# Kernel optimization log

Measured on AMD Instinct MI355X. Metric: run time of the kernel, lower is better.

Reference implementation:

```python
import jax, jax.numpy as jnp
import numpy as np

# Dims: B=batch, H=query heads, HKV=kv heads, T=query len, S=cache/key len, Dh=head dim
B, H, HKV, T, S, Dh = 2, 32, 8, 1024, 2048, 128
THRESH = 0.000488  # keep keys whose mean attention (over heads and queries) exceeds this


def setup_inputs() -> dict:
    key = jax.random.key(0)
    k1, k2, k3 = jax.random.split(key, 3)
    # attn_w emulates post-softmax attention probabilities: rows sum to 1 over key axis
    attn_w = jax.random.uniform(k1, (B, H, T, S), dtype=jnp.float32)
    attn_w = attn_w / attn_w.sum(axis=-1, keepdims=True)
    v = jax.random.normal(k2, (B, HKV, S, Dh), dtype=jnp.float32)
    w_o = jax.random.normal(k3, (H * Dh, H * Dh), dtype=jnp.float32) * 0.02  # o_proj weight (no bias, Mistral)
    return {"attn_w": attn_w, "v": v, "w_o": w_o}


def reference(attn_w, v, w_o):
    # keep = attn_w.mean(dim=(1,2)) > thresh  -> [B, S]
    keep = attn_w.mean(axis=(1, 2)) > THRESH
    pruned_weights = attn_w * keep[:, None, None, :].astype(attn_w.dtype)  # [B,H,T,S]
    # repeat_kv: [B,HKV,S,Dh] -> [B,H,S,Dh] via repeat_interleave on head axis
    groups = attn_w.shape[1] // v.shape[1]
    v_full = jnp.repeat(v, groups, axis=1)
    new_ctx = jnp.einsum('bhts,bhsd->bhtd', pruned_weights, v_full)  # [B,H,T,Dh]
    Bn, Hn, Tn, Dn = new_ctx.shape
    new_ctx = new_ctx.transpose(0, 2, 1, 3).reshape(Bn, Tn, Hn * Dn)  # [B,T,H*Dh]
    out = new_ctx @ w_o.T  # o_proj
    return (out, pruned_weights)
```

## Files before the change

kernel.cpp:

```cpp
#include <hip/hip_runtime.h>
#include <hip/hip_bf16.h>

#define B_ 2
#define H_ 32
#define HKV_ 8
#define T_ 1024
#define S_ 2048
#define DH_ 128
#define HD_ 4096
#define NROW_ 32768
#define THRESH_D 0.000488

typedef __attribute__((ext_vector_type(4))) float f32x4;
typedef __attribute__((ext_vector_type(8))) short bf16x8;

#define SCHED0() __builtin_amdgcn_sched_barrier(0)

__device__ __forceinline__ void gload_lds16(const void* g, void* l) {
  __builtin_amdgcn_global_load_lds(
      (const __attribute__((address_space(1))) void*)g,
      (__attribute__((address_space(3))) void*)l, 16, 0, 0);
}


__global__ void reduce_wo_k(const double* __restrict__ partial,
                            float* __restrict__ keep,
                            const float* __restrict__ w,
                            __hip_bfloat16* __restrict__ wb) {
  __shared__ double sh[4][64];
  if (blockIdx.x < 64) {
    int b = blockIdx.x >> 5;
    int s0 = (blockIdx.x & 31) * 64;
    int wv = threadIdx.x >> 6, l = threadIdx.x & 63;
    const double* p = partial + (size_t)b * 256 * S_ + s0 + l;
    double sum = 0.0;
    #pragma unroll 8
    for (int y = 0; y < 64; ++y) sum += p[(size_t)(wv * 64 + y) * S_];
    sh[wv][l] = sum;
    __syncthreads();
    if (wv == 0) {
      double t = (sh[0][l] + sh[1][l]) + (sh[2][l] + sh[3][l]);
      keep[b * S_ + s0 + l] = (t * (1.0 / 32768.0) > THRESH_D) ? 1.0f : 0.0f;
    }
  } else {
    size_t idx = ((size_t)(blockIdx.x - 64) * 256 + threadIdx.x) * 8;
    int n = (int)(idx >> 12);
    int k0 = (int)(idx & (HD_ - 1));
    float4 x = *(const float4*)(w + idx);
    float4 y = *(const float4*)(w + idx + 4);
    union { bf16x8 v8; __hip_bfloat16 h[8]; } u;
    u.h[0] = __float2bfloat16(x.x); u.h[1] = __float2bfloat16(x.y);
    u.h[2] = __float2bfloat16(x.z); u.h[3] = __float2bfloat16(x.w);
    u.h[4] = __float2bfloat16(y.x); u.h[5] = __float2bfloat16(y.y);
    u.h[6] = __float2bfloat16(y.z); u.h[7] = __float2bfloat16(y.w);
    int ksw = (k0 & ~63) | ((k0 ^ ((n & 7) << 3)) & 63);
    *(bf16x8*)(wb + (size_t)n * HD_ + ksw) = u.v8;
  }
}


#define BK2 64
#define NS2 64

__global__ __launch_bounds__(512) void gemm2_k(
    const __hip_bfloat16* __restrict__ Actx,
    const __hip_bfloat16* __restrict__ Bw,
    float* __restrict__ out) {
  __shared__ __align__(16) __hip_bfloat16 As[2][128 * BK2];
  __shared__ __align__(16) __hip_bfloat16 Bs[2][128 * BK2];
  int tid = threadIdx.x;
  int lg = ((blockIdx.x & 7) << 6) | (blockIdx.x >> 3);
  int n0 = (lg >> 4) * 128;
  int m0 = (lg & 15) * 128;
  const __hip_bfloat16* Ap = Actx + (size_t)m0 * HD_;
  const __hip_bfloat16* Bp = Bw + (size_t)n0 * HD_;
  int wave = tid >> 6, lane = tid & 63;
  int l16 = lane & 15, lk = lane >> 4;

  f32x4 acc[8];
  f32x4 z = {0.f, 0.f, 0.f, 0.f};
  #pragma unroll
  for (int n = 0; n < 8; ++n) acc[n] = z;

  auto issue = [&](int ks, int buf) {
    const __hip_bfloat16* ga = Ap + (size_t)(tid >> 3) * HD_ + ks * BK2 + (tid & 7) * 8;
    const __hip_bfloat16* gb = Bp + (size_t)(tid >> 3) * HD_ + ks * BK2 + (tid & 7) * 8;
    char* la = (char*)&As[buf][0] + tid * 16;
    char* lb = (char*)&Bs[buf][0] + tid * 16;
    gload_lds16(ga, la);
    gload_lds16(ga + (size_t)64 * HD_, la + 8192);
    gload_lds16(gb, lb);
    gload_lds16(gb + (size_t)64 * HD_, lb + 8192);
  };

  auto mfmaStep = [&](int buf) {
    char* ab = (char*)&As[buf][0];
    char* bb = (char*)&Bs[buf][0];
    #pragma unroll
    for (int kk = 0; kk < 2; ++kk) {
      int kb = kk * 64 + lk * 16;
      int ar = wave * 16 + l16;
      bf16x8 af = *(const bf16x8*)(ab + (ar * 128 + (kb ^ ((ar & 7) << 4))));
      #pragma unroll
      for (int n = 0; n < 8; ++n) {
        int br = n * 16 + l16;
        bf16x8 bf = *(const bf16x8*)(bb + (br * 128 + (kb ^ ((br & 7) << 4))));
        acc[n] = __builtin_amdgcn_mfma_f32_16x16x32_bf16(af, bf, acc[n], 0, 0, 0);
      }
    }
  };

  issue(0, 0);
  for (int ks = 0; ks < NS2; ++ks) {
    int cur = ks & 1;
    if (ks + 1 < NS2) issue(ks + 1, cur ^ 1);
    SCHED0();
    if (ks + 1 < NS2) {
      asm volatile("s_waitcnt vmcnt(4) lgkmcnt(0)" ::: "memory");
    } else {
      asm volatile("s_waitcnt vmcnt(0) lgkmcnt(0)" ::: "memory");
    }
    SCHED0();
    __builtin_amdgcn_s_barrier();
    SCHED0();
    mfmaStep(cur);
    SCHED0();
    __builtin_amdgcn_s_barrier();
    SCHED0();
  }

  #pragma unroll
  for (int n = 0; n < 8; ++n)
    #pragma unroll
    for (int r = 0; r < 4; ++r) {
      int row = m0 + wave * 16 + lk * 4 + r;
      int col = n0 + n * 16 + l16;
      out[(size_t)row * HD_ + col] = acc[n][r];
    }
}


__global__ __launch_bounds__(256) void colsumA_k(
    const float* __restrict__ attn, double* __restrict__ partial,
    __hip_bfloat16* __restrict__ abf) {
  int tid = threadIdx.x;
  int chunk = blockIdx.x;
  size_t base = (size_t)chunk * 128 * S_;
  const float* ap = attn + base;
  __hip_bfloat16* ob = abf + base;
  double a0 = 0, a1 = 0, a2 = 0, a3 = 0;
  double b0 = 0, b1 = 0, b2 = 0, b3 = 0;
  #pragma unroll 4
  for (int i = 0; i < 256; ++i) {
    size_t off = (size_t)i * 1024 + tid * 4;
    f32x4 vv = *(const f32x4*)(ap + off);
    int row = i >> 1;
    int s = ((i & 1) << 10) + tid * 4;
    int ssw = (s & ~63) | ((s ^ ((row & 7) << 3)) & 63);
    union { ushort4 u4; __hip_bfloat16 h[4]; } u;
    u.h[0] = __float2bfloat16(vv.x); u.h[1] = __float2bfloat16(vv.y);
    u.h[2] = __float2bfloat16(vv.z); u.h[3] = __float2bfloat16(vv.w);
    *(ushort4*)(ob + (size_t)row * S_ + ssw) = u.u4;
    if (i & 1) { b0 += vv.x; b1 += vv.y; b2 += vv.z; b3 += vv.w; }
    else       { a0 += vv.x; a1 += vv.y; a2 += vv.z; a3 += vv.w; }
  }
  double* o = partial + (size_t)chunk * S_ + tid * 4;
  o[0] = a0; o[1] = a1; o[2] = a2; o[3] = a3;
  double* o2 = partial + (size_t)chunk * S_ + 1024 + tid * 4;
  o2[0] = b0; o2[1] = b1; o2[2] = b2; o2[3] = b3;
}

__global__ void convert_vA_k(const float* __restrict__ v,
                             const float* __restrict__ keep,
                             __hip_bfloat16* __restrict__ vt) {
  __shared__ float tile[32][33];
  int bh = blockIdx.z;
  int b = bh >> 3;
  int s0 = blockIdx.x * 32, d0 = blockIdx.y * 32;
  const float* vp = v + (size_t)bh * (S_ * DH_);
  __hip_bfloat16* vtp = vt + (size_t)bh * (S_ * DH_);
  int tx = threadIdx.x, ty = threadIdx.y;
  for (int i = 0; i < 32; i += 8)
    tile[ty + i][tx] = vp[(size_t)(s0 + ty + i) * DH_ + d0 + tx];
  __syncthreads();
  int s = s0 + tx;
  float kv = keep[b * S_ + s];
  for (int i = 0; i < 32; i += 8) {
    int d = d0 + ty + i;
    int ssw = (s & ~63) | ((s ^ ((d & 7) << 3)) & 63);
    vtp[(size_t)d * S_ + ssw] = __float2bfloat16(tile[tx][ty + i] * kv);
  }
}

#define BK1 64
#define NS1 32

__global__ __launch_bounds__(512, 4) void prune_gemm1A_k(
    const __hip_bfloat16* __restrict__ abf, const float* __restrict__ keep,
    const __hip_bfloat16* __restrict__ vt, float* __restrict__ pruned,
    __hip_bfloat16* __restrict__ ctx) {
  __shared__ __align__(16) __hip_bfloat16 As[2][128 * BK1];
  __shared__ __align__(16) __hip_bfloat16 Bs[2][128 * BK1];
  __shared__ __align__(16) float ksh[S_];

  int tid = threadIdx.x;
  int lg = ((blockIdx.x & 7) << 6) | (blockIdx.x >> 3);
  int bh = lg >> 3;
  int t0 = (lg & 7) * 128;
  int b = bh >> 5, h = bh & 31, hkv = h >> 2;
  int rot = (lg * 17) & 31;
  const __hip_bfloat16* Ab = abf + ((size_t)bh * T_ + t0) * S_;
  float* P = pruned + ((size_t)bh * T_ + t0) * S_;
  const __hip_bfloat16* Bv = vt + (size_t)(b * HKV_ + hkv) * (DH_ * S_);
  const float* kp = keep + b * S_;

  int wave = tid >> 6, lane = tid & 63;
  int l16 = lane & 15, lk = lane >> 4;

  f32x4 acc[8];
  f32x4 z = {0.f, 0.f, 0.f, 0.f};
  #pragma unroll
  for (int n = 0; n < 8; ++n) acc[n] = z;

  auto col = [&](int j) { return (j + rot) & 31; };

  auto issueA = [&](int cks, int buf) {
    const __hip_bfloat16* g0 = Ab + (size_t)(tid >> 3) * S_ + cks * BK1 + (tid & 7) * 8;
    char* la = (char*)&As[buf][0] + tid * 16;
    gload_lds16(g0, la);
    gload_lds16(g0 + (size_t)64 * S_, la + 8192);
  };

  auto issueB = [&](int cks, int buf) {
    const __hip_bfloat16* g0 = Bv + (size_t)(tid >> 3) * S_ + cks * BK1 + (tid & 7) * 8;
    char* lb = (char*)&Bs[buf][0] + tid * 16;
    gload_lds16(g0, lb);
    gload_lds16(g0 + (size_t)64 * S_, lb + 8192);
  };

  auto mfmaStep = [&](int buf) {
    char* ab = (char*)&As[buf][0];
    char* bb = (char*)&Bs[buf][0];
    #pragma unroll
    for (int kk = 0; kk < 2; ++kk) {
      int kb = kk * 64 + lk * 16;
      int ar = wave * 16 + l16;
      bf16x8 af = *(const bf16x8*)(ab + (ar * 128 + (kb ^ ((ar & 7) << 4))));
      #pragma unroll
      for (int n = 0; n < 8; ++n) {
        int br = n * 16 + l16;
        bf16x8 bf = *(const bf16x8*)(bb + (br * 128 + (kb ^ ((br & 7) << 4))));
        acc[n] = __builtin_amdgcn_mfma_f32_16x16x32_bf16(af, bf, acc[n], 0, 0, 0);
      }
    }
  };

  auto prunedWrite = [&](int cks, int buf) {
    char* ab = (char*)&As[buf][0];
    union { bf16x8 v; unsigned int d[4]; } u0, u1;
    u0.v = *(const bf16x8*)(ab + tid * 16);
    u1.v = *(const bf16x8*)(ab + tid * 16 + 8192);
    int row0 = tid >> 3;
    int scol = cks * BK1 + (((tid & 7) * 8) ^ ((row0 & 7) << 3));
    f32x4 k0 = *(const f32x4*)&ksh[scol];
    f32x4 k1 = *(const f32x4*)&ksh[scol + 4];
    f32x4 p00, p01, p10, p11;
    p00.x = __uint_as_float(u0.d[0] << 16) * k0.x;
    p00.y = __uint_as_float(u0.d[0] & 0xFFFF0000u) * k0.y;
    p00.z = __uint_as_float(u0.d[1] << 16) * k0.z;
    p00.w = __uint_as_float(u0.d[1] & 0xFFFF0000u) * k0.w;
    p01.x = __uint_as_float(u0.d[2] << 16) * k1.x;
    p01.y = __uint_as_float(u0.d[2] & 0xFFFF0000u) * k1.y;
    p01.z = __uint_as_float(u0.d[3] << 16) * k1.z;
    p01.w = __uint_as_float(u0.d[3] & 0xFFFF0000u) * k1.w;
    p10.x = __uint_as_float(u1.d[0] << 16) * k0.x;
    p10.y = __uint_as_float(u1.d[0] & 0xFFFF0000u) * k0.y;
    p10.z = __uint_as_float(u1.d[1] << 16) * k0.z;
    p10.w = __uint_as_float(u1.d[1] & 0xFFFF0000u) * k0.w;
    p11.x = __uint_as_float(u1.d[2] << 16) * k1.x;
    p11.y = __uint_as_float(u1.d[2] & 0xFFFF0000u) * k1.y;
    p11.z = __uint_as_float(u1.d[3] << 16) * k1.z;
    p11.w = __uint_as_float(u1.d[3] & 0xFFFF0000u) * k1.w;
    float* gp0 = P + (size_t)row0 * S_ + scol;
    float* gp1 = P + (size_t)(row0 + 64) * S_ + scol;
    *(f32x4*)gp0 = p00; *(f32x4*)(gp0 + 4) = p01;
    *(f32x4*)gp1 = p10; *(f32x4*)(gp1 + 4) = p11;
  };

  gload_lds16(kp + tid * 4, (char*)ksh + tid * 16);
  issueA(col(0), 0);
  issueB(col(0), 0);
  SCHED0();
  asm volatile("s_waitcnt vmcnt(4)" ::: "memory");
  SCHED0();
  __builtin_amdgcn_s_barrier();
  SCHED0();

  for (int ks = 0; ks < NS1; ++ks) {
    int cur = ks & 1;
    if (ks + 1 < NS1) {
      issueA(col(ks + 1), cur ^ 1);
      issueB(col(ks + 1), cur ^ 1);
    }
    SCHED0();
    if (ks == 0 || ks == NS1 - 1) {
      asm volatile("s_waitcnt vmcnt(4) lgkmcnt(0)" ::: "memory");
    } else {
      asm volatile("s_waitcnt vmcnt(8) lgkmcnt(0)" ::: "memory");
    }
    SCHED0();
    __builtin_amdgcn_s_barrier();
    SCHED0();
    mfmaStep(cur);
    prunedWrite(col(ks), cur);
    SCHED0();
    __builtin_amdgcn_s_barrier();
    SCHED0();
  }

  #pragma unroll
  for (int n = 0; n < 8; ++n)
    #pragma unroll
    for (int r = 0; r < 4; ++r) {
      int trow = t0 + wave * 16 + lk * 4 + r;
      int rowm = b * T_ + trow;
      int kcol = h * DH_ + n * 16 + l16;
      int ksw = (kcol & ~63) | ((kcol ^ ((rowm & 7) << 3)) & 63);
      ctx[(size_t)rowm * HD_ + ksw] = __float2bfloat16(acc[n][r]);
    }
}


__global__ __launch_bounds__(256) void colsumB_k(
    const float* __restrict__ attn, double* __restrict__ partial) {
  int tid = threadIdx.x;
  int chunk = blockIdx.x;
  size_t base = (size_t)chunk * 128 * S_;
  const float* ap = attn + base;
  double a0 = 0, a1 = 0, a2 = 0, a3 = 0;
  double b0 = 0, b1 = 0, b2 = 0, b3 = 0;
  #pragma unroll 4
  for (int i = 0; i < 256; ++i) {
    size_t off = (size_t)i * 1024 + tid * 4;
    f32x4 vv = *(const f32x4*)(ap + off);
    if (i & 1) { b0 += vv.x; b1 += vv.y; b2 += vv.z; b3 += vv.w; }
    else       { a0 += vv.x; a1 += vv.y; a2 += vv.z; a3 += vv.w; }
  }
  double* o = partial + (size_t)chunk * S_ + tid * 4;
  o[0] = a0; o[1] = a1; o[2] = a2; o[3] = a3;
  double* o2 = partial + (size_t)chunk * S_ + 1024 + tid * 4;
  o2[0] = b0; o2[1] = b1; o2[2] = b2; o2[3] = b3;
}

__global__ void convert_vB_k(const float* __restrict__ v,
                             __hip_bfloat16* __restrict__ vt) {
  __shared__ float tile[32][33];
  int bh = blockIdx.z;
  int s0 = blockIdx.x * 32, d0 = blockIdx.y * 32;
  const float* vp = v + (size_t)bh * (S_ * DH_);
  __hip_bfloat16* vtp = vt + (size_t)bh * (S_ * DH_);
  int tx = threadIdx.x, ty = threadIdx.y;
  for (int i = 0; i < 32; i += 8)
    tile[ty + i][tx] = vp[(size_t)(s0 + ty + i) * DH_ + d0 + tx];
  __syncthreads();
  int s = s0 + tx;
  for (int i = 0; i < 32; i += 8) {
    int d = d0 + ty + i;
    int ssw = (s & ~63) | ((s ^ ((d & 7) << 3)) & 63);
    vtp[(size_t)d * S_ + ssw] = __float2bfloat16(tile[tx][ty + i]);
  }
}

__global__ __launch_bounds__(512, 4) void prune_gemm1B_k(
    const float* __restrict__ attn, const float* __restrict__ keep,
    const __hip_bfloat16* __restrict__ vt, float* __restrict__ pruned,
    __hip_bfloat16* __restrict__ ctx) {
  __shared__ __align__(16) __hip_bfloat16 As[2][128 * BK1];
  __shared__ __align__(16) __hip_bfloat16 Bs[2][128 * BK1];
  __shared__ __align__(16) float ksh[S_];

  int tid = threadIdx.x;
  int lg = ((blockIdx.x & 7) << 6) | (blockIdx.x >> 3);
  int bh = lg >> 3;
  int t0 = (lg & 7) * 128;
  int b = bh >> 5, h = bh & 31, hkv = h >> 2;
  int rot = (lg * 17) & 31;
  const float* A = attn + ((size_t)bh * T_ + t0) * S_;
  float* P = pruned + ((size_t)bh * T_ + t0) * S_;
  const __hip_bfloat16* Bv = vt + (size_t)(b * HKV_ + hkv) * (DH_ * S_);
  const float* kp = keep + b * S_;

  int arow = tid >> 2;
  int acol = (tid & 3) * 16;
  int wave = tid >> 6, lane = tid & 63;
  int l16 = lane & 15, lk = lane >> 4;

  f32x4 acc[8];
  f32x4 z = {0.f, 0.f, 0.f, 0.f};
  #pragma unroll
  for (int n = 0; n < 8; ++n) acc[n] = z;

  f32x4 areg0[4], areg1[4];

  auto col = [&](int j) { return (j + rot) & 31; };

  auto issueA = [&](int cks, f32x4* bank) {
    const float* ga = A + (size_t)arow * S_ + cks * BK1 + acol;
    #pragma unroll
    for (int j = 0; j < 4; ++j) bank[j] = *(const f32x4*)(ga + j * 4);
  };

  auto issueB = [&](int cks, int buf) {
    const __hip_bfloat16* g0 = Bv + (size_t)(tid >> 3) * S_ + cks * BK1 + (tid & 7) * 8;
    char* lb = (char*)&Bs[buf][0] + tid * 16;
    gload_lds16(g0, lb);
    gload_lds16(g0 + (size_t)64 * S_, lb + 8192);
  };

  auto stageA = [&](int cks, int buf, const f32x4* bank) {
    f32x4 p[4];
    #pragma unroll
    for (int j = 0; j < 4; ++j) {
      f32x4 kv = *(const f32x4*)&ksh[cks * BK1 + acol + j * 4];
      p[j] = bank[j] * kv;
    }
    float* gp = P + (size_t)arow * S_ + cks * BK1 + acol;
    #pragma unroll
    for (int j = 0; j < 4; ++j) *(f32x4*)(gp + j * 4) = p[j];
    union { bf16x8 v8; __hip_bfloat16 h[8]; } u0, u1;
    const float* pf = (const float*)&p[0];
    #pragma unroll
    for (int j = 0; j < 8; ++j) u0.h[j] = __float2bfloat16(pf[j]);
    #pragma unroll
    for (int j = 0; j < 8; ++j) u1.h[j] = __float2bfloat16(pf[8 + j]);
    char* ab = (char*)&As[buf][0];
    int base0 = arow * 128 + acol * 2;
    int sw = (arow & 7) << 4;
    *(bf16x8*)(ab + (base0 ^ sw)) = u0.v8;
    *(bf16x8*)(ab + ((base0 + 16) ^ sw)) = u1.v8;
  };

  auto mfmaStep = [&](int buf) {
    char* ab = (char*)&As[buf][0];
    char* bb = (char*)&Bs[buf][0];
    #pragma unroll
    for (int kk = 0; kk < 2; ++kk) {
      int kb = kk * 64 + lk * 16;
      int ar = wave * 16 + l16;
      bf16x8 af = *(const bf16x8*)(ab + (ar * 128 + (kb ^ ((ar & 7) << 4))));
      #pragma unroll
      for (int n = 0; n < 8; ++n) {
        int br = n * 16 + l16;
        bf16x8 bf = *(const bf16x8*)(bb + (br * 128 + (kb ^ ((br & 7) << 4))));
        acc[n] = __builtin_amdgcn_mfma_f32_16x16x32_bf16(af, bf, acc[n], 0, 0, 0);
      }
    }
  };

  gload_lds16(kp + tid * 4, (char*)ksh + tid * 16);
  issueB(col(0), 0);
  issueA(col(0), areg0);
  SCHED0();
  asm volatile("s_waitcnt vmcnt(6)" ::: "memory");
  SCHED0();
  __builtin_amdgcn_s_barrier();
  SCHED0();
  issueA(col(1), areg1);
  stageA(col(0), 0, areg0);

  for (int ks = 0; ks < NS1; ks += 2) {
    {
      if (ks + 1 < NS1) issueB(col(ks + 1), 1);
      if (ks + 2 < NS1) issueA(col(ks + 2), areg0);
      if (ks + 1 < NS1) stageA(col(ks + 1), 1, areg1);
      SCHED0();
      if (ks + 2 < NS1)      { asm volatile("s_waitcnt vmcnt(18) lgkmcnt(0)" ::: "memory"); }
      else if (ks + 1 < NS1) { asm volatile("s_waitcnt vmcnt(14) lgkmcnt(0)" ::: "memory"); }
      else                   { asm volatile("s_waitcnt vmcnt(4) lgkmcnt(0)" ::: "memory"); }
      SCHED0();
      __builtin_amdgcn_s_barrier();
      SCHED0();
      mfmaStep(0);
      SCHED0();
      __builtin_amdgcn_s_barrier();
      SCHED0();
    }
    {
      int ko = ks + 1;
      if (ko + 1 < NS1) issueB(col(ko + 1), 0);
      if (ko + 2 < NS1) issueA(col(ko + 2), areg1);
      if (ko + 1 < NS1) stageA(col(ko + 1), 0, areg0);
      SCHED0();
      if (ko + 2 < NS1)      { asm volatile("s_waitcnt vmcnt(18) lgkmcnt(0)" ::: "memory"); }
      else if (ko + 1 < NS1) { asm volatile("s_waitcnt vmcnt(14) lgkmcnt(0)" ::: "memory"); }
      else                   { asm volatile("s_waitcnt vmcnt(4) lgkmcnt(0)" ::: "memory"); }
      SCHED0();
      __builtin_amdgcn_s_barrier();
      SCHED0();
      mfmaStep(1);
      SCHED0();
      __builtin_amdgcn_s_barrier();
      SCHED0();
    }
  }

  #pragma unroll
  for (int n = 0; n < 8; ++n)
    #pragma unroll
    for (int r = 0; r < 4; ++r) {
      int trow = t0 + wave * 16 + lk * 4 + r;
      int rowm = b * T_ + trow;
      int kcol = h * DH_ + n * 16 + l16;
      int ksw = (kcol & ~63) | ((kcol ^ ((rowm & 7) << 3)) & 63);
      ctx[(size_t)rowm * HD_ + ksw] = __float2bfloat16(acc[n][r]);
    }
}


extern "C" void kernel_launch(void* const* d_in, const int* in_sizes, int n_in,
                              void* d_out, int out_size, void* d_ws, size_t ws_size,
                              hipStream_t stream) {
  const float* attn = (const float*)d_in[0];
  const float* v = (const float*)d_in[1];
  const float* w_o = (const float*)d_in[2];
  float* out = (float*)d_out;
  float* pruned = out + (size_t)B_ * T_ * HD_;

  char* ws = (char*)d_ws;
  size_t off = 0;
  double* partial = (double*)(ws + off); off += (size_t)B_ * 256 * S_ * 8;
  float* keep = (float*)(ws + off);      off += (size_t)B_ * S_ * 4;
  __hip_bfloat16* vt = (__hip_bfloat16*)(ws + off);
  off += (size_t)B_ * HKV_ * DH_ * S_ * 2;
  __hip_bfloat16* wo = (__hip_bfloat16*)(ws + off);
  off += (size_t)HD_ * HD_ * 2;
  __hip_bfloat16* ctx = (__hip_bfloat16*)(ws + off);
  off += (size_t)B_ * T_ * HD_ * 2;
  __hip_bfloat16* abf = (__hip_bfloat16*)(ws + off);
  size_t need_abf = off + (size_t)B_ * NROW_ * S_ * 2;

  bool bigws = (ws_size >= need_abf);
  int wo_grid = 64 + (HD_ * HD_) / (256 * 8);

  if (bigws) {
    colsumA_k<<<dim3(512), 256, 0, stream>>>(attn, partial, abf);
    reduce_wo_k<<<dim3(wo_grid), 256, 0, stream>>>(partial, keep, w_o, wo);
    convert_vA_k<<<dim3(S_ / 32, DH_ / 32, B_ * HKV_), dim3(32, 8), 0, stream>>>(v, keep, vt);
    prune_gemm1A_k<<<dim3(512), 512, 0, stream>>>(abf, keep, vt, pruned, ctx);
  } else {
    colsumB_k<<<dim3(512), 256, 0, stream>>>(attn, partial);
    reduce_wo_k<<<dim3(wo_grid), 256, 0, stream>>>(partial, keep, w_o, wo);
    convert_vB_k<<<dim3(S_ / 32, DH_ / 32, B_ * HKV_), dim3(32, 8), 0, stream>>>(v, vt);
    prune_gemm1B_k<<<dim3(512), 512, 0, stream>>>(attn, keep, vt, pruned, ctx);
  }
  gemm2_k<<<dim3(512), 512, 0, stream>>>(ctx, wo, out);

  (void)in_sizes; (void)n_in; (void)out_size; (void)ws_size;
}
```

Before: 448.5 us.

## Load attention A-operand directly into registers instead of staging through LDS

```diff
diff --git a/kernel.cpp b/kernel.cpp
--- a/kernel.cpp
+++ b/kernel.cpp
@@ -199,7 +199,6 @@
     const __hip_bfloat16* __restrict__ abf, const float* __restrict__ keep,
     const __hip_bfloat16* __restrict__ vt, float* __restrict__ pruned,
     __hip_bfloat16* __restrict__ ctx) {
-  __shared__ __align__(16) __hip_bfloat16 As[2][128 * BK1];
   __shared__ __align__(16) __hip_bfloat16 Bs[2][128 * BK1];
   __shared__ __align__(16) float ksh[S_];
 
@@ -209,27 +208,28 @@
   int t0 = (lg & 7) * 128;
   int b = bh >> 5, h = bh & 31, hkv = h >> 2;
   int rot = (lg * 17) & 31;
-  const __hip_bfloat16* Ab = abf + ((size_t)bh * T_ + t0) * S_;
+  const char* Ab = (const char*)(abf + ((size_t)bh * T_ + t0) * S_);
   float* P = pruned + ((size_t)bh * T_ + t0) * S_;
   const __hip_bfloat16* Bv = vt + (size_t)(b * HKV_ + hkv) * (DH_ * S_);
   const float* kp = keep + b * S_;
 
   int wave = tid >> 6, lane = tid & 63;
   int l16 = lane & 15, lk = lane >> 4;
+  int ar = wave * 16 + l16;
+  int prow = tid >> 3;
+  int afoff0 = (lk * 16) ^ ((ar & 7) << 4);
+  int afoff1 = (64 + lk * 16) ^ ((ar & 7) << 4);
+  int pwoff = (tid & 7) * 16;
 
   f32x4 acc[8];
   f32x4 z = {0.f, 0.f, 0.f, 0.f};
   #pragma unroll
   for (int n = 0; n < 8; ++n) acc[n] = z;
 
+  bf16x8 afA0, afA1, pwA0, pwA1;
+  bf16x8 afB0, afB1, pwB0, pwB1;
+
   auto col = [&](int j) { return (j + rot) & 31; };
-
-  auto issueA = [&](int cks, int buf) {
-    const __hip_bfloat16* g0 = Ab + (size_t)(tid >> 3) * S_ + cks * BK1 + (tid & 7) * 8;
-    char* la = (char*)&As[buf][0] + tid * 16;
-    gload_lds16(g0, la);
-    gload_lds16(g0 + (size_t)64 * S_, la + 8192);
-  };
 
   auto issueB = [&](int cks, int buf) {
     const __hip_bfloat16* g0 = Bv + (size_t)(tid >> 3) * S_ + cks * BK1 + (tid & 7) * 8;
@@ -238,14 +238,20 @@
     gload_lds16(g0 + (size_t)64 * S_, lb + 8192);
   };
 
-  auto mfmaStep = [&](int buf) {
-    char* ab = (char*)&As[buf][0];
+  auto prefA = [&](int cks, bf16x8& a0, bf16x8& a1, bf16x8& p0, bf16x8& p1) {
+    const char* tb = Ab + (size_t)cks * 128;
+    a0 = *(const bf16x8*)(tb + (size_t)ar * (2 * S_) + afoff0);
+    a1 = *(const bf16x8*)(tb + (size_t)ar * (2 * S_) + afoff1);
+    p0 = *(const bf16x8*)(tb + (size_t)prow * (2 * S_) + pwoff);
+    p1 = *(const bf16x8*)(tb + (size_t)(prow + 64) * (2 * S_) + pwoff);
+  };
+
+  auto mfmaStep = [&](int buf, bf16x8 a0, bf16x8 a1) {
     char* bb = (char*)&Bs[buf][0];
     #pragma unroll
     for (int kk = 0; kk < 2; ++kk) {
       int kb = kk * 64 + lk * 16;
-      int ar = wave * 16 + l16;
-      bf16x8 af = *(const bf16x8*)(ab + (ar * 128 + (kb ^ ((ar & 7) << 4))));
+      bf16x8 af = kk ? a1 : a0;
       #pragma unroll
       for (int n = 0; n < 8; ++n) {
         int br = n * 16 + l16;
@@ -255,13 +261,10 @@
     }
   };
 
-  auto prunedWrite = [&](int cks, int buf) {
-    char* ab = (char*)&As[buf][0];
+  auto prunedWrite = [&](int cks, bf16x8 p0v, bf16x8 p1v) {
     union { bf16x8 v; unsigned int d[4]; } u0, u1;
-    u0.v = *(const bf16x8*)(ab + tid * 16);
-    u1.v = *(const bf16x8*)(ab + tid * 16 + 8192);
-    int row0 = tid >> 3;
-    int scol = cks * BK1 + (((tid & 7) * 8) ^ ((row0 & 7) << 3));
+    u0.v = p0v; u1.v = p1v;
+    int scol = cks * BK1 + (((tid & 7) * 8) ^ ((prow & 7) << 3));
     f32x4 k0 = *(const f32x4*)&ksh[scol];
     f32x4 k1 = *(const f32x4*)&ksh[scol + 4];
     f32x4 p00, p01, p10, p11;
@@ -281,41 +284,56 @@
     p11.y = __uint_as_float(u1.d[2] & 0xFFFF0000u) * k1.y;
     p11.z = __uint_as_float(u1.d[3] << 16) * k1.z;
     p11.w = __uint_as_float(u1.d[3] & 0xFFFF0000u) * k1.w;
-    float* gp0 = P + (size_t)row0 * S_ + scol;
-    float* gp1 = P + (size_t)(row0 + 64) * S_ + scol;
+    float* gp0 = P + (size_t)prow * S_ + scol;
+    float* gp1 = P + (size_t)(prow + 64) * S_ + scol;
     *(f32x4*)gp0 = p00; *(f32x4*)(gp0 + 4) = p01;
     *(f32x4*)gp1 = p10; *(f32x4*)(gp1 + 4) = p11;
   };
 
   gload_lds16(kp + tid * 4, (char*)ksh + tid * 16);
-  issueA(col(0), 0);
   issueB(col(0), 0);
   SCHED0();
-  asm volatile("s_waitcnt vmcnt(4)" ::: "memory");
+  prefA(col(0), afA0, afA1, pwA0, pwA1);
+  SCHED0();
+  asm volatile("s_waitcnt vmcnt(6)" ::: "memory");
   SCHED0();
   __builtin_amdgcn_s_barrier();
   SCHED0();
 
-  for (int ks = 0; ks < NS1; ++ks) {
-    int cur = ks & 1;
-    if (ks + 1 < NS1) {
-      issueA(col(ks + 1), cur ^ 1);
-      issueB(col(ks + 1), cur ^ 1);
-    }
-    SCHED0();
-    if (ks == 0 || ks == NS1 - 1) {
-      asm volatile("s_waitcnt vmcnt(4) lgkmcnt(0)" ::: "memory");
-    } else {
-      asm volatile("s_waitcnt vmcnt(8) lgkmcnt(0)" ::: "memory");
-    }
-    SCHED0();
-    __builtin_amdgcn_s_barrier();
-    SCHED0();
-    mfmaStep(cur);
-    prunedWrite(col(ks), cur);
-    SCHED0();
-    __builtin_amdgcn_s_barrier();
-    SCHED0();
+  for (int ks = 0; ks < NS1; ks += 2) {
+    {
+      if (ks + 1 < NS1) issueB(col(ks + 1), 1);
+      SCHED0();
+      if (ks + 1 < NS1) prefA(col(ks + 1), afB0, afB1, pwB0, pwB1);
+      SCHED0();
+      if (ks == 0) { asm volatile("s_waitcnt vmcnt(10) lgkmcnt(0)" ::: "memory"); }
+      else         { asm volatile("s_waitcnt vmcnt(14) lgkmcnt(0)" ::: "memory"); }
+      SCHED0();
+      __builtin_amdgcn_s_barrier();
+      SCHED0();
+      mfmaStep(0, afA0, afA1);
+      prunedWrite(col(ks), pwA0, pwA1);
+      SCHED0();
+      __builtin_amdgcn_s_barrier();
+      SCHED0();
+    }
+    {
+      int ko = ks + 1;
+      if (ko + 1 < NS1) issueB(col(ko + 1), 0);
+      SCHED0();
+      if (ko + 1 < NS1) prefA(col(ko + 1), afA0, afA1, pwA0, pwA1);
+      SCHED0();
+      if (ko + 1 < NS1) { asm volatile("s_waitcnt vmcnt(14) lgkmcnt(0)" ::: "memory"); }
+      else              { asm volatile("s_waitcnt vmcnt(8) lgkmcnt(0)" ::: "memory"); }
+      SCHED0();
+      __builtin_amdgcn_s_barrier();
+      SCHED0();
+      mfmaStep(1, afB0, afB1);
+      prunedWrite(col(ko), pwB0, pwB1);
+      SCHED0();
+      __builtin_amdgcn_s_barrier();
+      SCHED0();
+    }
   }
 
   #pragma unroll
```

Measured after the change: 457.6 us. 2.0% more time.
